# Performance work log

Hardware: AMD Instinct MI355X
Metric: run time of the kernel (lower is better)

## Reference

```python
import jax, jax.numpy as jnp
import numpy as np
import math

S, B, D, H = 2048, 2, 1024, 16
DK = D // H

def setup_inputs() -> dict:
    key = jax.random.key(0)
    ks = jax.random.split(key, 32)
    f = lambda k, shape, s=1.0: jax.random.normal(k, shape, dtype=jnp.float32) * s
    inp = {
        'qx': f(ks[0], (S, B, D)),
        'kx': f(ks[1], (S, B, D)),
        'vx': f(ks[2], (S, B, D)),
        'qc': f(ks[3], (S, B, D)),
        'kc': f(ks[4], (S, B, D)),
    }
    w = 1.0 / math.sqrt(D)
    names = ['qx_lin', 'kx_lin', 'vx_lin', 'qc_lin', 'kc_lin', 'out_lin']
    for i, n in enumerate(names):
        inp['W_' + n] = f(ks[5 + 2 * i], (D, D), w)
        inp['b_' + n] = f(ks[6 + 2 * i], (D,), w)
    vnames = ['Vqx', 'Vqc', 'Vkx', 'Vkc']
    for i, n in enumerate(vnames):
        inp['W_' + n] = f(ks[17 + 2 * i], (D, 1), w)
        inp['b_' + n] = f(ks[18 + 2 * i], (1,), w)
    return inp

def _forward(qx, kx, vx, qc, kc,
             W_qx_lin, b_qx_lin, W_kx_lin, b_kx_lin, W_vx_lin, b_vx_lin,
             W_qc_lin, b_qc_lin, W_kc_lin, b_kc_lin, W_out_lin, b_out_lin,
             W_Vqx, b_Vqx, W_Vqc, b_Vqc, W_Vkx, b_Vkx, W_Vkc, b_Vkc):
    # [S,B,D] -> [B,S,D]
    qx = jnp.swapaxes(qx, 0, 1)
    kx = jnp.swapaxes(kx, 0, 1)
    vx = jnp.swapaxes(vx, 0, 1)
    qc = jnp.swapaxes(qc, 0, 1)
    kc = jnp.swapaxes(kc, 0, 1)
    bs = qx.shape[0]

    qx = qx @ W_qx_lin + b_qx_lin
    kx = kx @ W_kx_lin + b_kx_lin
    v = vx @ W_vx_lin + b_vx_lin
    qc = qc @ W_qc_lin + b_qc_lin
    kc = kc @ W_kc_lin + b_kc_lin

    lam_q = jax.nn.sigmoid((qx @ W_Vqx + b_Vqx) + (qc @ W_Vqc + b_Vqc))  # [B,S,1]
    lam_k = jax.nn.sigmoid((kx @ W_Vkx + b_Vkx) + (kc @ W_Vkc + b_Vkc))
    q = (1.0 - lam_q) * qx + lam_q * qc
    k = (1.0 - lam_k) * kx + lam_k * kc

    # [B,S,D] -> [B,H,S,dk]
    q = q.reshape(bs, -1, H, DK).transpose(0, 2, 1, 3)
    k = k.reshape(bs, -1, H, DK).transpose(0, 2, 1, 3)
    v = v.reshape(bs, -1, H, DK).transpose(0, 2, 1, 3)

    scores = jnp.einsum('bhqd,bhkd->bhqk', q, k) / math.sqrt(DK)
    attn = jax.nn.softmax(scores, axis=-1)  # dropout is identity in eval
    ctx = jnp.einsum('bhqk,bhkd->bhqd', attn, v)

    concat = ctx.transpose(0, 2, 1, 3).reshape(bs, -1, D)
    out = concat @ W_out_lin + b_out_lin
    return jnp.swapaxes(out, 0, 1)  # back to [S,B,D]

def reference(qx, kx, vx, qc, kc,
              W_qx_lin, b_qx_lin, W_kx_lin, b_kx_lin, W_vx_lin, b_vx_lin,
              W_qc_lin, b_qc_lin, W_kc_lin, b_kc_lin, W_out_lin, b_out_lin,
              W_Vqx, b_Vqx, W_Vqc, b_Vqc, W_Vkx, b_Vkx, W_Vkc, b_Vkc):
    return _forward(qx, kx, vx, qc, kc,
                    W_qx_lin, b_qx_lin, W_kx_lin, b_kx_lin, W_vx_lin, b_vx_lin,
                    W_qc_lin, b_qc_lin, W_kc_lin, b_kc_lin, W_out_lin, b_out_lin,
                    W_Vqx, b_Vqx, W_Vqc, b_Vqc, W_Vkx, b_Vkx, W_Vkc, b_Vkc)
```

## Files before the change

kernel.cpp:

```cpp
#include <hip/hip_runtime.h>
#include <math.h>

typedef unsigned short u16;
typedef __attribute__((ext_vector_type(8))) short short8;
typedef __attribute__((ext_vector_type(4))) float floatx4;
typedef __attribute__((ext_vector_type(4))) unsigned short ushort4v;
typedef __attribute__((ext_vector_type(2))) unsigned int uint2v;

__device__ __forceinline__ float bf2f(u16 x) {
    union { unsigned int u; float f; } v; v.u = ((unsigned int)x) << 16; return v.f;
}
__device__ __forceinline__ u16 f2bf(float f) {
    union { float f; unsigned int u; } v; v.f = f;
    unsigned int r = v.u + 0x7fffu + ((v.u >> 16) & 1u);
    return (u16)(r >> 16);
}
__device__ __forceinline__ unsigned int pk2bf(float a, float b) {
#if __has_builtin(__builtin_amdgcn_cvt_pk_bf16_f32)
    auto r = __builtin_amdgcn_cvt_pk_bf16_f32(a, b);
    union { decltype(r) v; unsigned int u; } cv; cv.v = r; return cv.u;
#else
    return (unsigned int)f2bf(a) | ((unsigned int)f2bf(b) << 16);
#endif
}
__device__ __forceinline__ float fexp2(float x) {
#if __has_builtin(__builtin_amdgcn_exp2f)
    return __builtin_amdgcn_exp2f(x);
#else
    return exp2f(x);
#endif
}

__device__ __forceinline__ void swap32(unsigned int& x0, unsigned int& x1, int lane) {
#if __has_builtin(__builtin_amdgcn_permlane32_swap)
    (void)lane;
    auto r = __builtin_amdgcn_permlane32_swap((int)x0, (int)x1, false, false);
    x0 = (unsigned int)r[0]; x1 = (unsigned int)r[1];
#else
    const bool hi = (lane & 32) != 0;
    const unsigned int s = hi ? x0 : x1;
    const unsigned int rr = (unsigned int)__shfl_xor((int)s, 32, 64);
    const unsigned int n0 = hi ? rr : x0;
    const unsigned int n1 = hi ? x1 : rr;
    x0 = n0; x1 = n1;
#endif
}
__device__ __forceinline__ void swap16(unsigned int& x0, unsigned int& x1, int lane) {
#if __has_builtin(__builtin_amdgcn_permlane16_swap)
    (void)lane;
    auto r = __builtin_amdgcn_permlane16_swap((int)x0, (int)x1, false, false);
    x0 = (unsigned int)r[0]; x1 = (unsigned int)r[1];
#else
    const bool hi = (lane & 16) != 0;
    const unsigned int s = hi ? x0 : x1;
    const unsigned int rr = (unsigned int)__shfl_xor((int)s, 16, 64);
    const unsigned int n0 = hi ? rr : x0;
    const unsigned int n1 = hi ? x1 : rr;
    x0 = n0; x1 = n1;
#endif
}

__device__ __forceinline__ void g2l16(const u16* g, u16* l) {
    __builtin_amdgcn_global_load_lds(
        (const __attribute__((address_space(1))) void*)g,
        (__attribute__((address_space(3))) void*)l, 16, 0, 0);
}

struct WFuseJobs { const float* W[4]; const float* wv[4]; const float* bl[4];
                   float* out[4]; float* bdot; };

__global__ __launch_bounds__(256) void wfuse(WFuseJobs wf) {
    const int z = blockIdx.y;
    const float* W = wf.W[z];
    const float* wv = wf.wv[z];
    float* out = wf.out[z];
    const int t = threadIdx.x;
    const int lane = t & 63, w = t >> 6;
#pragma unroll
    for (int i = 0; i < 4; i++) {
        const int row = blockIdx.x * 16 + w * 4 + i;
        const float* Wr = W + (size_t)row * 1024 + lane * 16;
        const float* vr = wv + lane * 16;
        float p = 0.f;
#pragma unroll
        for (int c = 0; c < 4; c++) {
            const floatx4 a = *(const floatx4*)(Wr + c * 4);
            const floatx4 b = *(const floatx4*)(vr + c * 4);
            p += a[0] * b[0] + a[1] * b[1] + a[2] * b[2] + a[3] * b[3];
        }
#pragma unroll
        for (int m = 1; m <= 32; m <<= 1) p += __shfl_xor(p, m);
        if (lane == 0) out[row] = p;
    }
    if (blockIdx.x == 0) {
        const floatx4 bb = *(const floatx4*)(wf.bl[z] + t * 4);
        const floatx4 vv = *(const floatx4*)(wv + t * 4);
        float p = bb[0] * vv[0] + bb[1] * vv[1] + bb[2] * vv[2] + bb[3] * vv[3];
#pragma unroll
        for (int m = 1; m <= 32; m <<= 1) p += __shfl_xor(p, m);
        __shared__ float red[4];
        if ((t & 63) == 0) red[t >> 6] = p;
        __syncthreads();
        if (t == 0) wf.bdot[z] = red[0] + red[1] + red[2] + red[3];
    }
}

struct GCJobs {
    const float* xa[3]; const float* xc[3];
    const float* w1[3]; const float* w2[3];
    const float* bdot;
    const float* sA[3]; const float* sB[3];
    float* lamout[3];
    u16* dst[3];
};

__global__ __launch_bounds__(256) void gatecast(GCJobs gj) {
    const int z = blockIdx.y;
    const int row = blockIdx.x;
    const int t = threadIdx.x;
    const size_t off = (size_t)row * 1024 + t * 4;
    const floatx4 a = *(const floatx4*)(gj.xa[z] + off);

    if (z == 2) {
        ushort4v o;
        const unsigned int lo = pk2bf(a[0], a[1]);
        const unsigned int hi = pk2bf(a[2], a[3]);
        o[0] = (u16)(lo & 0xffff); o[1] = (u16)(lo >> 16);
        o[2] = (u16)(hi & 0xffff); o[3] = (u16)(hi >> 16);
        *(ushort4v*)(gj.dst[2] + (size_t)row * 1024 + t * 4) = o;
        return;
    }

    const floatx4 c  = *(const floatx4*)(gj.xc[z] + off);
    const floatx4 w1 = *(const floatx4*)(gj.w1[z] + t * 4);
    const floatx4 w2 = *(const floatx4*)(gj.w2[z] + t * 4);
    float p = 0.f;
#pragma unroll
    for (int j = 0; j < 4; j++) p += a[j] * w1[j] + c[j] * w2[j];
#pragma unroll
    for (int m = 1; m <= 32; m <<= 1) p += __shfl_xor(p, m);
    __shared__ float red[4];
    if ((t & 63) == 0) red[t >> 6] = p;
    __syncthreads();
    const float x = red[0] + red[1] + red[2] + red[3]
                  + gj.bdot[2 * z] + gj.bdot[2 * z + 1]
                  + gj.sA[z][0] + gj.sB[z][0];
    const float lam = 1.f / (1.f + exp2f(-x * 1.44269504f));
    if (t == 0) gj.lamout[z][row] = lam;
    const float oml = 1.f - lam;

    u16* d = gj.dst[z] + (size_t)row * 2048 + t * 4;
    ushort4v o1, o2;
    {
        const unsigned int lo = pk2bf(oml * a[0], oml * a[1]);
        const unsigned int hi = pk2bf(oml * a[2], oml * a[3]);
        o1[0] = (u16)(lo & 0xffff); o1[1] = (u16)(lo >> 16);
        o1[2] = (u16)(hi & 0xffff); o1[3] = (u16)(hi >> 16);
    }
    {
        const unsigned int lo = pk2bf(lam * c[0], lam * c[1]);
        const unsigned int hi = pk2bf(lam * c[2], lam * c[3]);
        o2[0] = (u16)(lo & 0xffff); o2[1] = (u16)(lo >> 16);
        o2[2] = (u16)(hi & 0xffff); o2[3] = (u16)(hi >> 16);
    }
    *(ushort4v*)d = o1;
    *(ushort4v*)(d + 1024) = o2;
}

struct WTJobs { const float* src[6]; u16* dst[6]; int stride[6]; int koff[6]; };

__global__ __launch_bounds__(256) void wtrans(WTJobs wj) {
    __shared__ float tile[32][33];
    const int z = blockIdx.z;
    const float* W = wj.src[z];
    u16* Wt = wj.dst[z];
    const int stride = wj.stride[z], koff = wj.koff[z];
    const int n0 = blockIdx.x * 32, k0 = blockIdx.y * 32;
    const int tx = threadIdx.x & 31, ty = threadIdx.x >> 5;
#pragma unroll
    for (int i = 0; i < 4; i++)
        tile[ty + i * 8][tx] = W[(size_t)(k0 + ty + i * 8) * 1024 + n0 + tx];
    __syncthreads();
#pragma unroll
    for (int i = 0; i < 4; i++)
        Wt[(size_t)(n0 + ty + i * 8) * stride + koff + k0 + tx] = f2bf(tile[tx][ty + i * 8]);
}

__global__ __launch_bounds__(256) void vtrans(const u16* __restrict__ V,
                                              u16* __restrict__ Vtg) {
    __shared__ u16 tile[32][34];
    const int bh = blockIdx.z, b = bh >> 4, h = bh & 15;
    const int base = b * 1024 + h * 64;
    const int s0 = blockIdx.x * 32, d0 = blockIdx.y * 32;
    const int tx = threadIdx.x & 31, ty = threadIdx.x >> 5;
#pragma unroll
    for (int i = 0; i < 4; i++)
        tile[ty + i * 8][tx] = V[(size_t)(s0 + ty + i * 8) * 2048 + base + d0 + tx];
    __syncthreads();
#pragma unroll
    for (int i = 0; i < 4; i++)
        Vtg[((size_t)bh * 64 + d0 + ty + i * 8) * 2048 + s0 + tx] = tile[tx][ty + i * 8];
}

struct PJob {
    const u16* A; const u16* Bt; int K;
    const float* biasA; const float* biasC; const float* lam;
    u16* out; float* outf; float scale;
};
struct PJobs { PJob j[4]; };

__global__ __launch_bounds__(256, 3) void projall(PJobs jobs) {
    __shared__ __align__(16) u16 As[2][128 * 32];
    __shared__ __align__(16) u16 Bs[2][128 * 32];
    const int nj = gridDim.z;
    const int bid = blockIdx.x + 8 * (blockIdx.y + 32 * blockIdx.z);
    const int sw = (bid & 7) * (32 * nj) + (bid >> 3);
    const PJob jb = jobs.j[sw >> 8];
    const int K = jb.K;
    const int m0 = ((sw >> 3) & 31) * 128;
    const int n0 = (sw & 7) * 128;
    const int t = threadIdx.x;
    const int lane = t & 63;
    const int wid = t >> 6;
    const int wm = wid >> 1, wn = wid & 1;
    const int qd = lane >> 4, lm = lane & 15;

    const floatx4 zero4 = {0.f, 0.f, 0.f, 0.f};
    floatx4 acc[4][4];
#pragma unroll
    for (int i = 0; i < 4; i++)
#pragma unroll
        for (int j2 = 0; j2 < 4; j2++) acc[i][j2] = zero4;

    const int srow = t >> 2;
    const int su = (t & 3) ^ (srow & 3);
    const u16* Ap = jb.A + (size_t)(m0 + srow) * K + su * 8;
    const u16* Bp = jb.Bt + (size_t)(n0 + srow) * K + su * 8;

#define PSTAGE(BUF, KOFF) do {                                         \
        g2l16(Ap + (KOFF),                   &As[BUF][t * 8]);         \
        g2l16(Ap + (KOFF) + (size_t)64 * K,  &As[BUF][2048 + t * 8]);  \
        g2l16(Bp + (KOFF),                   &Bs[BUF][t * 8]);         \
        g2l16(Bp + (KOFF) + (size_t)64 * K,  &Bs[BUF][2048 + t * 8]);  \
    } while (0)

    PSTAGE(0, 0);
    __syncthreads();
    int cur = 0;
    const int ua = (qd ^ (lm & 3)) << 3;
    for (int k0 = 0; k0 < K; k0 += 32) {
        if (k0 + 32 < K) PSTAGE(cur ^ 1, k0 + 32);

        short8 af[4], bfg[4];
#pragma unroll
        for (int i = 0; i < 4; i++) {
            af[i]  = *(const short8*)&As[cur][(wm * 64 + i * 16 + lm) * 32 + ua];
            bfg[i] = *(const short8*)&Bs[cur][(wn * 64 + i * 16 + lm) * 32 + ua];
        }
#pragma unroll
        for (int i = 0; i < 4; i++)
#pragma unroll
            for (int j2 = 0; j2 < 4; j2++)
                acc[i][j2] = __builtin_amdgcn_mfma_f32_16x16x32_bf16(af[i], bfg[j2], acc[i][j2], 0, 0, 0);

        __syncthreads();
        cur ^= 1;
    }
#undef PSTAGE

#pragma unroll
    for (int i = 0; i < 4; i++) {
        const int mb = m0 + wm * 64 + i * 16 + qd * 4;
        float lamv[4];
        if (jb.lam) {
#pragma unroll
            for (int r = 0; r < 4; r++) lamv[r] = jb.lam[mb + r];
        }
#pragma unroll
        for (int j2 = 0; j2 < 4; j2++) {
            const int col = n0 + wn * 64 + j2 * 16 + lm;
            const float bA = jb.biasA[col];
            if (jb.outf) {
#pragma unroll
                for (int r = 0; r < 4; r++)
                    jb.outf[(size_t)(mb + r) * 1024 + col] = acc[i][j2][r] + bA;
            } else if (jb.lam) {
                const float dB = jb.biasC[col] - bA;
#pragma unroll
                for (int r = 0; r < 4; r++)
                    jb.out[(size_t)(mb + r) * 1024 + col] =
                        f2bf((acc[i][j2][r] + bA + lamv[r] * dB) * jb.scale);
            } else {
#pragma unroll
                for (int r = 0; r < 4; r++)
                    jb.out[(size_t)(mb + r) * 1024 + col] =
                        f2bf((acc[i][j2][r] + bA) * jb.scale);
            }
        }
    }
}

__global__ __launch_bounds__(256, 4) void attn6(
    const u16* __restrict__ Q, const u16* __restrict__ Kk,
    const u16* __restrict__ Vtg, float* __restrict__ ctxp,
    float* __restrict__ lp) {
    __shared__ __align__(16) u16 SB[16384];

    const int bid = blockIdx.x + 16 * (blockIdx.y + 32 * blockIdx.z);
    const int sw = (bid & 7) * 128 + (bid >> 3);
    const int qt = sw & 15;
    const int bh = (sw >> 4) & 31;
    const int sp = sw >> 9;
    const int b = bh >> 4, h = bh & 15;
    const int hb = b * 1024 + h * 64;

    const int t = threadIdx.x, lane = t & 63, w = t >> 6;
    const int qd = lane >> 4, lm = lane & 15;
    const int q0w = qt * 128 + w * 32;

    short8 qf[2][2];
#pragma unroll
    for (int qh = 0; qh < 2; qh++) {
        const u16* qr = Q + (size_t)(q0w + qh * 16 + lm) * 2048 + hb;
#pragma unroll
        for (int c = 0; c < 2; c++)
            qf[qh][c] = *(const short8*)(qr + c * 32 + qd * 8);
    }

    const floatx4 zero4 = {0.f, 0.f, 0.f, 0.f};
    floatx4 ctx[2][4];
#pragma unroll
    for (int qh = 0; qh < 2; qh++)
#pragma unroll
        for (int g = 0; g < 4; g++) ctx[qh][g] = zero4;
    floatx4 accL[2] = {zero4, zero4};

    union { unsigned int u[4]; short8 s; } ov;
    ov.u[0] = ov.u[1] = ov.u[2] = ov.u[3] = 0x3F803F80u;
    const short8 onesb = ov.s;

    const int rl = lane >> 3;
    const int cuz = (lane & 7) ^ rl;
    const u16* kp = Kk + (size_t)(sp * 1024 + w * 16 + rl) * 2048 + hb + cuz * 8;
    const u16* vp = Vtg + ((size_t)bh * 64 + w * 16 + rl) * 2048 + sp * 1024 + cuz * 8;
    u16* kd = &SB[(w * 16) * 64];
    u16* vd = &SB[4096 + (w * 16) * 64];

    const int rdA = lm * 64 + ((qd ^ (lm & 7)) << 3);
    const int rdB = rdA ^ 32;

#define STAGE(BUF) do {                                             \
        g2l16(kp,            kd + (BUF) * 8192);                    \
        g2l16(kp + 8 * 2048, kd + (BUF) * 8192 + 8 * 64);           \
        g2l16(vp,            vd + (BUF) * 8192);                    \
        g2l16(vp + 8 * 2048, vd + (BUF) * 8192 + 8 * 64);           \
        kp += 64 * 2048; vp += 64;                                  \
    } while (0)

#define COMPUTE(BUF) do {                                                          \
        short8 pa[2][2];                                                           \
        _Pragma("unroll")                                                          \
        for (int gp = 0; gp < 2; gp++) {                                           \
            unsigned int pw[2][2][2];                                              \
            _Pragma("unroll")                                                      \
            for (int g0 = 0; g0 < 2; g0++) {                                       \
                const int g = gp * 2 + g0;                                         \
                const short8 kf0 = *(const short8*)&SB[(BUF) * 8192 + g * 1024 + rdA]; \
                const short8 kf1 = *(const short8*)&SB[(BUF) * 8192 + g * 1024 + rdB]; \
                _Pragma("unroll")                                                  \
                for (int qh = 0; qh < 2; qh++) {                                   \
                    floatx4 st = zero4;                                            \
                    st = __builtin_amdgcn_mfma_f32_16x16x32_bf16(kf0, qf[qh][0], st, 0, 0, 0); \
                    st = __builtin_amdgcn_mfma_f32_16x16x32_bf16(kf1, qf[qh][1], st, 0, 0, 0); \
                    const float e0 = fexp2(st[0]), e1 = fexp2(st[1]);              \
                    const float e2 = fexp2(st[2]), e3 = fexp2(st[3]);              \
                    pw[qh][g0][0] = pk2bf(e0, e1);                                 \
                    pw[qh][g0][1] = pk2bf(e2, e3);                                 \
                }                                                                  \
            }                                                                      \
            _Pragma("unroll")                                                      \
            for (int qh = 0; qh < 2; qh++) {                                       \
                unsigned int a0 = pw[qh][0][0], b0 = pw[qh][1][0];                 \
                unsigned int a1 = pw[qh][0][1], b1 = pw[qh][1][1];                 \
                swap32(a0, b0, lane); swap32(a1, b1, lane);                        \
                swap16(a0, b0, lane); swap16(a1, b1, lane);                        \
                union { unsigned int u[4]; short8 s; } cv;                         \
                cv.u[0] = a0; cv.u[1] = a1; cv.u[2] = b0; cv.u[3] = b1;            \
                pa[qh][gp] = cv.s;                                                 \
            }                                                                      \
        }                                                                          \
        __builtin_amdgcn_s_setprio(1);                                             \
        _Pragma("unroll")                                                          \
        for (int g = 0; g < 4; g++) {                                              \
            const short8 vb0 = *(const short8*)&SB[(BUF) * 8192 + 4096 + g * 1024 + rdA]; \
            const short8 vb1 = *(const short8*)&SB[(BUF) * 8192 + 4096 + g * 1024 + rdB]; \
            _Pragma("unroll")                                                      \
            for (int qh = 0; qh < 2; qh++) {                                       \
                ctx[qh][g] = __builtin_amdgcn_mfma_f32_16x16x32_bf16(pa[qh][0], vb0, ctx[qh][g], 0, 0, 0); \
                ctx[qh][g] = __builtin_amdgcn_mfma_f32_16x16x32_bf16(pa[qh][1], vb1, ctx[qh][g], 0, 0, 0); \
            }                                                                      \
        }                                                                          \
        _Pragma("unroll")                                                          \
        for (int qh = 0; qh < 2; qh++) {                                           \
            accL[qh] = __builtin_amdgcn_mfma_f32_16x16x32_bf16(pa[qh][0], onesb, accL[qh], 0, 0, 0); \
            accL[qh] = __builtin_amdgcn_mfma_f32_16x16x32_bf16(pa[qh][1], onesb, accL[qh], 0, 0, 0); \
        }                                                                          \
        __builtin_amdgcn_s_setprio(0);                                             \
    } while (0)

    STAGE(0);
#pragma unroll 1
    for (int it = 0; it < 8; it++) {
        __syncthreads();
        STAGE(1);
        COMPUTE(0);
        __syncthreads();
        if (it < 7) STAGE(0);
        COMPUTE(1);
    }
#undef STAGE
#undef COMPUTE

    float* cbase = ctxp + (size_t)sp * 4194304;
#pragma unroll
    for (int qh = 0; qh < 2; qh++) {
        if (lm == 0) {
#pragma unroll
            for (int r = 0; r < 4; r++)
                lp[(size_t)sp * 65536 + bh * 2048 + q0w + qh * 16 + qd * 4 + r] = accL[qh][r];
        }
#pragma unroll
        for (int r = 0; r < 4; r++) {
            const int srow = q0w + qh * 16 + qd * 4 + r;
            float* orow = cbase + (size_t)srow * 2048 + hb;
#pragma unroll
            for (int g = 0; g < 4; g++)
                orow[g * 16 + lm] = ctx[qh][g][r];
        }
    }
}

__global__ __launch_bounds__(256) void merge(const float* __restrict__ ctxp,
                                             const float* __restrict__ lp,
                                             u16* __restrict__ out) {
    const size_t idx = ((size_t)blockIdx.x * 256 + threadIdx.x) * 4;
    const floatx4 a = *(const floatx4*)(ctxp + idx);
    const floatx4 c = *(const floatx4*)(ctxp + 4194304 + idx);
    const int srow = (int)(idx >> 11);
    const int rem = (int)(idx & 2047);
    const int bh = rem >> 6;
    const float l = lp[bh * 2048 + srow] + lp[65536 + bh * 2048 + srow];
    const float inv = 1.0f / l;
    ushort4v o;
    const unsigned int lo = pk2bf((a[0] + c[0]) * inv, (a[1] + c[1]) * inv);
    const unsigned int hi = pk2bf((a[2] + c[2]) * inv, (a[3] + c[3]) * inv);
    o[0] = (u16)(lo & 0xffff); o[1] = (u16)(lo >> 16);
    o[2] = (u16)(hi & 0xffff); o[3] = (u16)(hi >> 16);
    *(ushort4v*)(out + idx) = o;
}

extern "C" void kernel_launch(void* const* d_in, const int* in_sizes, int n_in,
                              void* d_out, int out_size, void* d_ws, size_t ws_size,
                              hipStream_t stream) {
    const float* qx = (const float*)d_in[0];
    const float* kx = (const float*)d_in[1];
    const float* vx = (const float*)d_in[2];
    const float* qc = (const float*)d_in[3];
    const float* kc = (const float*)d_in[4];
    const float* W_qx = (const float*)d_in[5];   const float* b_qx = (const float*)d_in[6];
    const float* W_kx = (const float*)d_in[7];   const float* b_kx = (const float*)d_in[8];
    const float* W_vx = (const float*)d_in[9];   const float* b_vx = (const float*)d_in[10];
    const float* W_qc = (const float*)d_in[11];  const float* b_qc = (const float*)d_in[12];
    const float* W_kc = (const float*)d_in[13];  const float* b_kc = (const float*)d_in[14];
    const float* W_out = (const float*)d_in[15]; const float* b_out = (const float*)d_in[16];
    const float* W_Vqx = (const float*)d_in[17]; const float* b_Vqx = (const float*)d_in[18];
    const float* W_Vqc = (const float*)d_in[19]; const float* b_Vqc = (const float*)d_in[20];
    const float* W_Vkx = (const float*)d_in[21]; const float* b_Vkx = (const float*)d_in[22];
    const float* W_Vkc = (const float*)d_in[23]; const float* b_Vkc = (const float*)d_in[24];

    char* ws = (char*)d_ws;
    const size_t MB = 1048576;
    u16* Aq  = (u16*)ws;
    u16* Ak  = (u16*)(ws + 16 * MB);
    u16* Av  = (u16*)(ws + 32 * MB);
    u16* Wtq = (u16*)(ws + 40 * MB);
    u16* Wtk = (u16*)(ws + 44 * MB);
    u16* Wtv = (u16*)(ws + 48 * MB);
    u16* Wto = (u16*)(ws + 50 * MB);
    u16* Pv    = (u16*)(ws + 52 * MB);
    u16* qg    = (u16*)(ws + 60 * MB);
    u16* kg    = (u16*)(ws + 68 * MB);
    u16* ctxbf = (u16*)(ws + 76 * MB);
    float* wfused = (float*)(ws + 84 * MB);
    float* bdot   = (float*)(ws + 84 * MB + 16384);
    float* lam    = (float*)(ws + 84 * MB + 16384 + 256);
    float* l_part = (float*)(ws + 84 * MB + 16384 + 256 + 32768);
    float* ctxp = (float*)ws;
    u16* Vtg    = (u16*)(ws + 32 * MB);

    WFuseJobs wf;
    wf.W[0] = W_qx; wf.wv[0] = W_Vqx; wf.bl[0] = b_qx; wf.out[0] = wfused;
    wf.W[1] = W_qc; wf.wv[1] = W_Vqc; wf.bl[1] = b_qc; wf.out[1] = wfused + 1024;
    wf.W[2] = W_kx; wf.wv[2] = W_Vkx; wf.bl[2] = b_kx; wf.out[2] = wfused + 2048;
    wf.W[3] = W_kc; wf.wv[3] = W_Vkc; wf.bl[3] = b_kc; wf.out[3] = wfused + 3072;
    wf.bdot = bdot;
    wfuse<<<dim3(64, 4), 256, 0, stream>>>(wf);

    GCJobs gj;
    gj.xa[0] = qx; gj.xc[0] = qc; gj.w1[0] = wfused;        gj.w2[0] = wfused + 1024;
    gj.sA[0] = b_Vqx; gj.sB[0] = b_Vqc; gj.lamout[0] = lam;        gj.dst[0] = Aq;
    gj.xa[1] = kx; gj.xc[1] = kc; gj.w1[1] = wfused + 2048; gj.w2[1] = wfused + 3072;
    gj.sA[1] = b_Vkx; gj.sB[1] = b_Vkc; gj.lamout[1] = lam + 4096; gj.dst[1] = Ak;
    gj.xa[2] = vx; gj.xc[2] = nullptr; gj.w1[2] = nullptr; gj.w2[2] = nullptr;
    gj.sA[2] = nullptr; gj.sB[2] = nullptr; gj.lamout[2] = nullptr; gj.dst[2] = Av;
    gj.bdot = bdot;
    gatecast<<<dim3(4096, 3), 256, 0, stream>>>(gj);

    WTJobs wj;
    wj.src[0] = W_qx; wj.dst[0] = Wtq; wj.stride[0] = 2048; wj.koff[0] = 0;
    wj.src[1] = W_qc; wj.dst[1] = Wtq; wj.stride[1] = 2048; wj.koff[1] = 1024;
    wj.src[2] = W_kx; wj.dst[2] = Wtk; wj.stride[2] = 2048; wj.koff[2] = 0;
    wj.src[3] = W_kc; wj.dst[3] = Wtk; wj.stride[3] = 2048; wj.koff[3] = 1024;
    wj.src[4] = W_vx; wj.dst[4] = Wtv; wj.stride[4] = 1024; wj.koff[4] = 0;
    wj.src[5] = W_out; wj.dst[5] = Wto; wj.stride[5] = 1024; wj.koff[5] = 0;
    wtrans<<<dim3(32, 32, 6), 256, 0, stream>>>(wj);

    const float QSCALE = 0.18033688011112042f;
    PJobs pj;
    pj.j[0].A = Aq; pj.j[0].Bt = Wtq; pj.j[0].K = 2048;
    pj.j[0].biasA = b_qx; pj.j[0].biasC = b_qc; pj.j[0].lam = lam;
    pj.j[0].out = qg; pj.j[0].outf = nullptr; pj.j[0].scale = QSCALE;
    pj.j[1].A = Ak; pj.j[1].Bt = Wtk; pj.j[1].K = 2048;
    pj.j[1].biasA = b_kx; pj.j[1].biasC = b_kc; pj.j[1].lam = lam + 4096;
    pj.j[1].out = kg; pj.j[1].outf = nullptr; pj.j[1].scale = 1.0f;
    pj.j[2].A = Av; pj.j[2].Bt = Wtv; pj.j[2].K = 1024;
    pj.j[2].biasA = b_vx; pj.j[2].biasC = nullptr; pj.j[2].lam = nullptr;
    pj.j[2].out = Pv; pj.j[2].outf = nullptr; pj.j[2].scale = 1.0f;
    pj.j[3] = pj.j[2];
    projall<<<dim3(8, 32, 3), 256, 0, stream>>>(pj);

    vtrans<<<dim3(64, 2, 32), 256, 0, stream>>>(Pv, Vtg);

    attn6<<<dim3(16, 32, 2), 256, 0, stream>>>(qg, kg, Vtg, ctxp, l_part);

    merge<<<4096, 256, 0, stream>>>(ctxp, l_part, ctxbf);

    PJobs po;
    po.j[0].A = ctxbf; po.j[0].Bt = Wto; po.j[0].K = 1024;
    po.j[0].biasA = b_out; po.j[0].biasC = nullptr; po.j[0].lam = nullptr;
    po.j[0].out = nullptr; po.j[0].outf = (float*)d_out; po.j[0].scale = 1.0f;
    po.j[1] = po.j[0]; po.j[2] = po.j[0]; po.j[3] = po.j[0];
    projall<<<dim3(8, 32, 1), 256, 0, stream>>>(po);
}
```

Baseline: 334.2 us.

## Use 256x256 tiled 512-thread GEMM kernel for fused QKV projections

Adds a new projection kernel with 256x256 output tiles, BK=64, 8 waves per block and XOR-swizzled LDS staging, and uses it for the three input projections instead of the 128x128 projall kernel. Larger tiles raise arithmetic intensity and cut global and LDS traffic per MFMA. It also uses s_setprio around MFMA bursts. The cost is far fewer blocks (192 versus 768), which may underfill the GPU's CUs, plus higher register and LDS use (128KB LDS per block).

```diff
diff --git a/kernel.cpp b/kernel.cpp
--- a/kernel.cpp
+++ b/kernel.cpp
@@ -208,6 +208,114 @@
     u16* out; float* outf; float scale;
 };
 struct PJobs { PJob j[4]; };
+
+__global__ __launch_bounds__(512, 2) void proj256(PJobs jobs) {
+    __shared__ __align__(16) u16 As[2][256 * 64];
+    __shared__ __align__(16) u16 Bs[2][256 * 64];
+
+    const int nj = gridDim.z;
+    const int bid = blockIdx.x + 4 * (blockIdx.y + 16 * blockIdx.z);
+    const int sw = (bid & 7) * (8 * nj) + (bid >> 3);
+    const PJob jb = jobs.j[sw >> 6];
+    const int r = sw & 63;
+    const int m0 = (r >> 2) * 256;
+    const int n0 = (r & 3) * 256;
+    const int K = jb.K;
+
+    const int t = threadIdx.x;
+    const int lane = t & 63;
+    const int wv = t >> 6;
+    const int wm = wv >> 2, wn = wv & 3;
+    const int qd = lane >> 4, lm = lane & 15;
+
+    const floatx4 zero4 = {0.f, 0.f, 0.f, 0.f};
+    floatx4 acc[8][4];
+#pragma unroll
+    for (int i = 0; i < 8; i++)
+#pragma unroll
+        for (int j = 0; j < 4; j++) acc[i][j] = zero4;
+
+    const int srow = t >> 3;
+    const int su = (t & 7) ^ (srow & 7);
+    const u16* Ap = jb.A + (size_t)(m0 + srow) * K + su * 8;
+    const u16* Bp = jb.Bt + (size_t)(n0 + srow) * K + su * 8;
+
+#define ST256(BUF, KO) do {                                                  \
+        _Pragma("unroll")                                                    \
+        for (int s = 0; s < 4; s++) {                                        \
+            g2l16(Ap + (KO) + (size_t)(s * 64) * K, &As[BUF][s * 4096 + t * 8]); \
+            g2l16(Bp + (KO) + (size_t)(s * 64) * K, &Bs[BUF][s * 4096 + t * 8]); \
+        }                                                                    \
+    } while (0)
+
+    const int aRowBase = (wm * 128 + lm) * 64;
+    const int bRowBase = (wn * 64 + lm) * 64;
+    const int u0 = (qd ^ (lm & 7)) << 3;
+    const int u1 = ((4 + qd) ^ (lm & 7)) << 3;
+
+    ST256(0, 0);
+    const int ntiles = K >> 6;
+#pragma unroll 1
+    for (int kt = 0; kt < ntiles; kt++) {
+        const int buf = kt & 1;
+        __syncthreads();
+        if (kt + 1 < ntiles) ST256(buf ^ 1, (kt + 1) * 64);
+
+        const u16* Ab = &As[buf][0];
+        const u16* Bb = &Bs[buf][0];
+
+        short8 bf[4][2];
+#pragma unroll
+        for (int j = 0; j < 4; j++) {
+            bf[j][0] = *(const short8*)&Bb[bRowBase + j * 16 * 64 + u0];
+            bf[j][1] = *(const short8*)&Bb[bRowBase + j * 16 * 64 + u1];
+        }
+#pragma unroll
+        for (int i = 0; i < 8; i++) {
+            const short8 af0 = *(const short8*)&Ab[aRowBase + i * 16 * 64 + u0];
+            const short8 af1 = *(const short8*)&Ab[aRowBase + i * 16 * 64 + u1];
+            __builtin_amdgcn_s_setprio(1);
+#pragma unroll
+            for (int j = 0; j < 4; j++) {
+                acc[i][j] = __builtin_amdgcn_mfma_f32_16x16x32_bf16(af0, bf[j][0], acc[i][j], 0, 0, 0);
+                acc[i][j] = __builtin_amdgcn_mfma_f32_16x16x32_bf16(af1, bf[j][1], acc[i][j], 0, 0, 0);
+            }
+            __builtin_amdgcn_s_setprio(0);
+        }
+    }
+#undef ST256
+
+#pragma unroll
+    for (int i = 0; i < 8; i++) {
+        const int mb = m0 + wm * 128 + i * 16 + qd * 4;
+        float lamv[4];
+        if (jb.lam) {
+#pragma unroll
+            for (int rr = 0; rr < 4; rr++) lamv[rr] = jb.lam[mb + rr];
+        }
+#pragma unroll
+        for (int j = 0; j < 4; j++) {
+            const int col = n0 + wn * 64 + j * 16 + lm;
+            const float bA = jb.biasA[col];
+            if (jb.outf) {
+#pragma unroll
+                for (int rr = 0; rr < 4; rr++)
+                    jb.outf[(size_t)(mb + rr) * 1024 + col] = acc[i][j][rr] + bA;
+            } else if (jb.lam) {
+                const float dB = jb.biasC[col] - bA;
+#pragma unroll
+                for (int rr = 0; rr < 4; rr++)
+                    jb.out[(size_t)(mb + rr) * 1024 + col] =
+                        f2bf((acc[i][j][rr] + bA + lamv[rr] * dB) * jb.scale);
+            } else {
+#pragma unroll
+                for (int rr = 0; rr < 4; rr++)
+                    jb.out[(size_t)(mb + rr) * 1024 + col] =
+                        f2bf((acc[i][j][rr] + bA) * jb.scale);
+            }
+        }
+    }
+}
 
 __global__ __launch_bounds__(256, 3) void projall(PJobs jobs) {
     __shared__ __align__(16) u16 As[2][128 * 32];
@@ -537,7 +645,7 @@
     pj.j[2].biasA = b_vx; pj.j[2].biasC = nullptr; pj.j[2].lam = nullptr;
     pj.j[2].out = Pv; pj.j[2].outf = nullptr; pj.j[2].scale = 1.0f;
     pj.j[3] = pj.j[2];
-    projall<<<dim3(8, 32, 3), 256, 0, stream>>>(pj);
+    proj256<<<dim3(4, 16, 3), 512, 0, stream>>>(pj);
 
     vtrans<<<dim3(64, 2, 32), 256, 0, stream>>>(Pv, Vtg);
 
```

Result: slower. 344.6 us (+3.1%).
